# Optimization experiments

Measured on AMD Instinct MI355X. Metric: run time of the kernel, lower is better.

Reference implementation:

```python
import jax, jax.numpy as jnp
import numpy as np

SOFTCAP = 30.0

def setup_inputs() -> dict:
    key = jax.random.key(0)
    ks = jax.random.split(key, 5)
    T, D, F, E = 8192, 2048, 4096, 8
    s_in = 1.0 / np.sqrt(D)
    s_mid = 1.0 / np.sqrt(F)
    return {
        "hidden_states": jax.random.normal(ks[0], (T, D), jnp.float32),
        "gate_w": jax.random.normal(ks[1], (D, E), jnp.float32) * s_in,
        "w_gate": jax.random.normal(ks[2], (E, D, F), jnp.float32) * s_in,
        "w_up": jax.random.normal(ks[3], (E, D, F), jnp.float32) * s_in,
        "w_down": jax.random.normal(ks[4], (E, F, D), jnp.float32) * s_mid,
        "top_k": 2,
    }

def reference(hidden_states, gate_w, w_gate, w_up, w_down, top_k):
    x = hidden_states
    T = x.shape[0]
    # --- router: fp32 gate, tanh softcap, softmax ---
    logits = x.astype(jnp.float32) @ gate_w                      # [T, E]
    logits = jnp.tanh(logits / SOFTCAP) * SOFTCAP
    probs = jax.nn.softmax(logits, axis=-1)                      # [T, E]
    # --- top-k selection (weights are the softmax probs, no renorm) ---
    weights, idx = jax.lax.top_k(probs, top_k)                   # [T, k]
    combine = jnp.zeros_like(probs).at[jnp.arange(T)[:, None], idx].set(
        weights.astype(probs.dtype))                              # [T, E]
    combine = combine.astype(x.dtype)
    # --- expert MLPs: gelu(x@w_gate) * (x@w_up) @ w_down, scan over E ---
    def step(acc, ewts):
        wg, wu, wd, c = ewts                                     # [D,F],[D,F],[F,D],[T]
        h = jax.nn.gelu(x @ wg) * (x @ wu)                       # [T, F]
        return acc + c[:, None] * (h @ wd), None
    out, _ = jax.lax.scan(step, jnp.zeros_like(x),
                          (w_gate, w_up, w_down, combine.T))
    return out
```

## Files before the change

kernel.cpp:

```cpp
#include <hip/hip_runtime.h>
#include <hip/hip_bf16.h>
#include <cstdint>
#include <cstddef>

#define TNUM 8192
#define DDIM 2048
#define FDIM 4096
#define NEXP 8

typedef __attribute__((ext_vector_type(4))) float f32x4;
typedef __attribute__((ext_vector_type(4))) unsigned u32x4;
typedef __attribute__((ext_vector_type(8))) short s16x8;
typedef __attribute__((ext_vector_type(8))) __bf16 bf16x8v;

__device__ inline f32x4 mfma16(s16x8 a, s16x8 b, f32x4 c) {
  return __builtin_amdgcn_mfma_f32_16x16x32_bf16(
      __builtin_bit_cast(bf16x8v, a), __builtin_bit_cast(bf16x8v, b), c, 0, 0, 0);
}

__device__ inline unsigned short bf16r(float f) {
  union { float f; unsigned u; } x; x.f = f;
  unsigned r = x.u + 0x7fffu + ((x.u >> 16) & 1u);
  return (unsigned short)(r >> 16);
}

__device__ inline unsigned pk2(float a, float b) {
  __hip_bfloat162 h = __float22bfloat162_rn(make_float2(a, b));
  unsigned r;
  __builtin_memcpy(&r, &h, 4);
  return r;
}

typedef const __attribute__((address_space(1))) void* gp_t;
typedef __attribute__((address_space(3))) void* lp_t;
__device__ inline void gl16(const void* g, void* l) {
  __builtin_amdgcn_global_load_lds((gp_t)g, (lp_t)l, 16, 0, 0);
}

#define FENCE asm volatile("" ::: "memory")

__global__ __launch_bounds__(256) void k_router(
    const float* __restrict__ x, const float* __restrict__ gw,
    int* __restrict__ top_idx, float* __restrict__ top_w, int* __restrict__ counts) {
  __shared__ float gwT[NEXP][DDIM];
  const int tid = threadIdx.x;
  for (int i = tid; i < NEXP * DDIM; i += 256) {
    int d = i >> 3, e = i & 7;
    gwT[e][d] = gw[i];
  }
  __syncthreads();
  const int lane = tid & 63;
  const int t = blockIdx.x * 4 + (tid >> 6);
  const float4* xr = (const float4*)(x + (size_t)t * DDIM);
  double acc[NEXP];
#pragma unroll
  for (int e = 0; e < NEXP; e++) acc[e] = 0.0;
  for (int d4 = lane; d4 < DDIM / 4; d4 += 64) {
    float4 xv = xr[d4];
#pragma unroll
    for (int e = 0; e < NEXP; e++) {
      float4 gv = *(const float4*)&gwT[e][d4 * 4];
      acc[e] += (double)xv.x * gv.x + (double)xv.y * gv.y +
                (double)xv.z * gv.z + (double)xv.w * gv.w;
    }
  }
#pragma unroll
  for (int e = 0; e < NEXP; e++) {
    double v = acc[e];
#pragma unroll
    for (int s = 32; s > 0; s >>= 1) v += __shfl_xor(v, s);
    acc[e] = v;
  }
  if (lane == 0) {
    int i0 = 0; double b0 = acc[0];
#pragma unroll
    for (int e = 1; e < NEXP; e++) if (acc[e] > b0) { b0 = acc[e]; i0 = e; }
    int i1 = (i0 == 0) ? 1 : 0; double b1 = acc[i1];
#pragma unroll
    for (int e = 0; e < NEXP; e++) {
      if (e == i0 || e == i1) continue;
      if (acc[e] > b1) { b1 = acc[e]; i1 = e; }
    }
    float lc[NEXP]; float mx = -1e30f;
#pragma unroll
    for (int e = 0; e < NEXP; e++) {
      lc[e] = tanhf((float)(acc[e] * (1.0 / 30.0))) * 30.0f;
      mx = lc[e] > mx ? lc[e] : mx;
    }
    float s = 0.0f;
#pragma unroll
    for (int e = 0; e < NEXP; e++) { lc[e] = expf(lc[e] - mx); s += lc[e]; }
    float inv = 1.0f / s;
    top_idx[t * 2] = i0; top_idx[t * 2 + 1] = i1;
    top_w[t * 2] = lc[i0] * inv; top_w[t * 2 + 1] = lc[i1] * inv;
    atomicAdd(&counts[i0], 1);
    atomicAdd(&counts[i1], 1);
  }
}

__global__ void k_scan(const int* __restrict__ counts, int* __restrict__ offs,
                       int* __restrict__ cursor) {
  if (threadIdx.x == 0) {
    int s = 0;
    for (int e = 0; e < NEXP; e++) { offs[e] = s; cursor[e] = s; s += counts[e]; }
    offs[NEXP] = s;
  }
}

__global__ void k_scatter(const int* __restrict__ top_idx, const float* __restrict__ top_w,
                          int* __restrict__ cursor, int* __restrict__ perm_tok,
                          float* __restrict__ perm_w) {
  int t = blockIdx.x * 256 + threadIdx.x;
#pragma unroll
  for (int k = 0; k < 2; k++) {
    int e = top_idx[t * 2 + k];
    int pos = atomicAdd(&cursor[e], 1);
    perm_tok[pos] = t;
    perm_w[pos] = top_w[t * 2 + k];
  }
}

__global__ void k_cast(const float* __restrict__ x, unsigned short* __restrict__ xb) {
  size_t i = ((size_t)blockIdx.x * 256 + threadIdx.x) * 8;
  f32x4 a = *(const f32x4*)(x + i);
  f32x4 b = *(const f32x4*)(x + i + 4);
  u32x4 v;
  v[0] = pk2(a[0], a[1]); v[1] = pk2(a[2], a[3]);
  v[2] = pk2(b[0], b[1]); v[3] = pk2(b[2], b[3]);
  *(u32x4*)(xb + i) = v;
}

__global__ __launch_bounds__(256) void k_convT(
    const float* __restrict__ src, unsigned short* __restrict__ dst,
    int K, int N, int cmap) {
  __shared__ char ct[8192];
  const int e = blockIdx.z;
  const float* src_e = src + (size_t)e * K * N;
  const int nout = cmap ? 2 * N : N;
  unsigned short* dst_e = dst + (size_t)e * nout * K;
  const int k0 = blockIdx.y * 64, n0 = blockIdx.x * 64;
  const int tid = threadIdx.x;
#pragma unroll
  for (int i = 0; i < 4; i++) {
    int idx = tid + i * 256;
    int kr = idx >> 4, f4 = idx & 15;
    f32x4 v = *(const f32x4*)(src_e + (size_t)(k0 + kr) * N + n0 + f4 * 4);
#pragma unroll
    for (int j = 0; j < 4; j++) {
      int n = f4 * 4 + j;
      *(unsigned short*)(ct + n * 128 + ((kr * 2) ^ ((n & 7) << 4))) = bf16r(v[j]);
    }
  }
  __syncthreads();
#pragma unroll
  for (int i = 0; i < 2; i++) {
    int s = tid + i * 256;
    int n = s >> 3, ks = s & 7;
    int gn = n0 + n;
    int cd = cmap ? (((gn >> 4) << 5) + (gn & 15) + (cmap == 2 ? 16 : 0)) : gn;
    s16x8 val = *(const s16x8*)(ct + n * 128 + ((ks * 16) ^ ((n & 7) << 4)));
    *(s16x8*)(dst_e + (size_t)cd * K + k0 + ks * 8) = val;
  }
}

#define STG_A(KK, TN)                                                          \
  {                                                                            \
    char* d_ = lds + ((TN) & 1) * 65536 + (KK) * 16384 + wid * 2048;           \
    gl16(spA[0] + (size_t)(TN) * 128 + (KK) * 64, d_);                         \
    gl16(spA[1] + (size_t)(TN) * 128 + (KK) * 64, d_ + 1024);                  \
  }
#define STG_B(KK, TN)                                                          \
  {                                                                            \
    char* d_ = lds + ((TN) & 1) * 65536 + 32768 + (KK) * 16384 + wid * 2048;   \
    gl16(spB[0] + (size_t)(TN) * 128 + (KK) * 64, d_);                         \
    gl16(spB[1] + (size_t)(TN) * 128 + (KK) * 64, d_ + 1024);                  \
  }

#define VMC(N) asm volatile("s_waitcnt vmcnt(" #N ")" ::: "memory")

#define RGN(KK, TN, MORE)                                                      \
  {                                                                            \
    char* Aq_ = lds + ((TN) & 1) * 65536 + (KK) * 16384;                       \
    char* Bq_ = Aq_ + 32768;                                                   \
    s16x8 a_[8];                                                               \
    _Pragma("unroll") for (int mi = 0; mi < 8; mi++)                           \
      a_[mi] = *(const s16x8*)(Aq_ + (wr * 128 + mi * 16 + l15) * 64 + sl16);  \
    s16x8 b0_ = *(const s16x8*)(Bq_ + (wc * 64 + l15) * 64 + sl16);            \
    s16x8 b1_ = *(const s16x8*)(Bq_ + (wc * 64 + 16 + l15) * 64 + sl16);       \
    if (MORE) { STG_A(KK, (TN) + 1); }                                         \
    __builtin_amdgcn_s_setprio(1);                                             \
    _Pragma("unroll") for (int mi = 0; mi < 8; mi++) {                         \
      acc[mi][0] = mfma16(a_[mi], b0_, acc[mi][0]);                            \
      acc[mi][1] = mfma16(a_[mi], b1_, acc[mi][1]);                            \
    }                                                                          \
    __builtin_amdgcn_s_setprio(0);                                             \
    s16x8 b2_ = *(const s16x8*)(Bq_ + (wc * 64 + 32 + l15) * 64 + sl16);       \
    s16x8 b3_ = *(const s16x8*)(Bq_ + (wc * 64 + 48 + l15) * 64 + sl16);       \
    if (MORE) { STG_B(KK, (TN) + 1); }                                         \
    __builtin_amdgcn_s_setprio(1);                                             \
    _Pragma("unroll") for (int mi = 0; mi < 8; mi++) {                         \
      acc[mi][2] = mfma16(a_[mi], b2_, acc[mi][2]);                            \
      acc[mi][3] = mfma16(a_[mi], b3_, acc[mi][3]);                            \
    }                                                                          \
    __builtin_amdgcn_s_setprio(0);                                             \
  }

__global__ __launch_bounds__(512, 2) void k_mlp1(
    const unsigned short* __restrict__ xb, const unsigned short* __restrict__ wguT,
    const int* __restrict__ perm_tok, const int* __restrict__ offs,
    unsigned short* __restrict__ H) {
  extern __shared__ char lds[];
  const int e = blockIdx.z;
  const int off = offs[e], cnt = offs[e + 1] - off;
  const int nb = blockIdx.x * 256;
  const unsigned short* wgu_e = wguT + (size_t)e * 2 * DDIM * FDIM;
  const int tid = threadIdx.x;
  const int lane = tid & 63;
  const int wid = tid >> 6;
  const int wr = wid >> 2, wc = wid & 3;
  const int l15 = lane & 15, lk = lane >> 4;
  const int sl16 = (lk ^ ((l15 >> 1) & 3)) * 16;
  const int g16 = ((lane & 3) ^ ((lane >> 3) & 3)) * 16;
  const int NT = DDIM / 64;

#pragma unroll 1
  for (int mt = blockIdx.y; mt * 256 < cnt; mt += 8) {
    const char* spA[2];
    const char* spB[2];
#pragma unroll
    for (int c = 0; c < 2; c++) {
      int r = wid * 32 + c * 16 + (lane >> 2);
      int gm = mt * 256 + r;
      if (gm >= cnt) gm = cnt - 1;
      spA[c] = (const char*)(xb + (size_t)perm_tok[off + gm] * DDIM) + g16;
      spB[c] = (const char*)(wgu_e + (size_t)(nb + r) * DDIM) + g16;
    }
    f32x4 acc[8][4];
#pragma unroll
    for (int mi = 0; mi < 8; mi++)
#pragma unroll
      for (int ni = 0; ni < 4; ni++) acc[mi][ni] = f32x4{0.f, 0.f, 0.f, 0.f};

    STG_A(0, 0) STG_B(0, 0) STG_A(1, 0) STG_B(1, 0)
#pragma unroll 1
    for (int t = 0; t < NT; t++) {
      const bool more = (t + 1) < NT;
      VMC(4);
      FENCE;
      __builtin_amdgcn_s_barrier();
      FENCE;
      RGN(0, t, more)
      if (more) { VMC(4); } else { VMC(0); }
      FENCE;
      __builtin_amdgcn_s_barrier();
      FENCE;
      RGN(1, t, more)
    }

#pragma unroll
    for (int am = 0; am < 8; am++) {
      int rb = wr * 128 + am * 16 + lk * 4;
#pragma unroll
      for (int j = 0; j < 4; j++) {
        int gm = mt * 256 + rb + j;
        if (gm < cnt) {
          unsigned short* hrow = H + (size_t)(off + gm) * FDIM;
#pragma unroll
          for (int ni = 0; ni < 4; ni += 2) {
            int jj = (nb >> 4) + wc * 4 + ni;
            int hc = ((jj >> 1) << 4) + l15;
            float g = acc[am][ni][j];
            float u = acc[am][ni + 1][j];
            float x3 = g * g * g;
            float gl = 0.5f * g * (1.0f + tanhf(0.7978845608f * (g + 0.044715f * x3)));
            hrow[hc] = bf16r(gl * u);
          }
        }
      }
    }
  }
}

__global__ __launch_bounds__(512, 2) void k_mlp2(
    const unsigned short* __restrict__ H, const unsigned short* __restrict__ wdT,
    const int* __restrict__ perm_tok, const float* __restrict__ perm_w,
    const int* __restrict__ offs, float* __restrict__ out) {
  extern __shared__ char lds[];
  const int e = blockIdx.z;
  const int off = offs[e], cnt = offs[e + 1] - off;
  const int nb = blockIdx.x * 256;
  const unsigned short* wd_e = wdT + (size_t)e * FDIM * DDIM;
  const int tid = threadIdx.x;
  const int lane = tid & 63;
  const int wid = tid >> 6;
  const int wr = wid >> 2, wc = wid & 3;
  const int l15 = lane & 15, lk = lane >> 4;
  const int sl16 = (lk ^ ((l15 >> 1) & 3)) * 16;
  const int g16 = ((lane & 3) ^ ((lane >> 3) & 3)) * 16;
  const int NT = FDIM / 64;

#pragma unroll 1
  for (int mt = blockIdx.y; mt * 256 < cnt; mt += 8) {
    const char* spA[2];
    const char* spB[2];
#pragma unroll
    for (int c = 0; c < 2; c++) {
      int r = wid * 32 + c * 16 + (lane >> 2);
      int gm = mt * 256 + r;
      if (gm >= cnt) gm = cnt - 1;
      spA[c] = (const char*)(H + (size_t)(off + gm) * FDIM) + g16;
      spB[c] = (const char*)(wd_e + (size_t)(nb + r) * FDIM) + g16;
    }
    f32x4 acc[8][4];
#pragma unroll
    for (int mi = 0; mi < 8; mi++)
#pragma unroll
      for (int ni = 0; ni < 4; ni++) acc[mi][ni] = f32x4{0.f, 0.f, 0.f, 0.f};

    STG_A(0, 0) STG_B(0, 0) STG_A(1, 0) STG_B(1, 0)
#pragma unroll 1
    for (int t = 0; t < NT; t++) {
      const bool more = (t + 1) < NT;
      VMC(4);
      FENCE;
      __builtin_amdgcn_s_barrier();
      FENCE;
      RGN(0, t, more)
      if (more) { VMC(4); } else { VMC(0); }
      FENCE;
      __builtin_amdgcn_s_barrier();
      FENCE;
      RGN(1, t, more)
    }

#pragma unroll
    for (int am = 0; am < 8; am++) {
      int rb = wr * 128 + am * 16 + lk * 4;
#pragma unroll
      for (int j = 0; j < 4; j++) {
        int gm = mt * 256 + rb + j;
        if (gm < cnt) {
          int tok = perm_tok[off + gm];
          float w = perm_w[off + gm];
          float* orow = out + (size_t)tok * DDIM + nb + wc * 64 + l15;
#pragma unroll
          for (int ni = 0; ni < 4; ni++) atomicAdd(&orow[ni * 16], w * acc[am][ni][j]);
        }
      }
    }
  }
}

extern "C" void kernel_launch(void* const* d_in, const int* in_sizes, int n_in,
                              void* d_out, int out_size, void* d_ws, size_t ws_size,
                              hipStream_t stream) {
  const float* x = (const float*)d_in[0];
  const float* gw = (const float*)d_in[1];
  const float* wgate = (const float*)d_in[2];
  const float* wup = (const float*)d_in[3];
  const float* wdown = (const float*)d_in[4];
  float* out = (float*)d_out;

  const size_t XB_B = 33554432;
  const size_t H_B = 134217728;
  const size_t WGU_B = 268435456;
  const size_t WD_B = 134217728;

  char* ws = (char*)d_ws;
  unsigned short* xb = (unsigned short*)ws;
  unsigned short* H = (unsigned short*)(ws + XB_B);
  unsigned short* wguT = (unsigned short*)(ws + XB_B + H_B);
  unsigned short* wdT = (unsigned short*)(ws + XB_B + H_B + WGU_B);
  char* meta = ws + XB_B + H_B + WGU_B + WD_B;
  int* counts = (int*)(meta);
  int* offs = (int*)(meta + 64);
  int* cursor = (int*)(meta + 128);
  int* top_idx = (int*)(meta + 256);
  float* top_w = (float*)(meta + 256 + 65536);
  int* perm_tok = (int*)(meta + 256 + 131072);
  float* perm_w = (float*)(meta + 256 + 196608);

  (void)hipFuncSetAttribute((const void*)k_mlp1,
                            hipFuncAttributeMaxDynamicSharedMemorySize, 131072);
  (void)hipFuncSetAttribute((const void*)k_mlp2,
                            hipFuncAttributeMaxDynamicSharedMemorySize, 131072);

  (void)hipMemsetAsync(counts, 0, 64, stream);
  (void)hipMemsetAsync(d_out, 0, (size_t)TNUM * DDIM * 4, stream);
  k_router<<<TNUM / 4, 256, 0, stream>>>(x, gw, top_idx, top_w, counts);
  k_scan<<<1, 64, 0, stream>>>(counts, offs, cursor);
  k_scatter<<<TNUM / 256, 256, 0, stream>>>(top_idx, top_w, cursor, perm_tok, perm_w);
  k_cast<<<(TNUM * DDIM / 8) / 256, 256, 0, stream>>>(x, xb);
  k_convT<<<dim3(FDIM / 64, DDIM / 64, NEXP), 256, 0, stream>>>(wgate, wguT, DDIM, FDIM, 1);
  k_convT<<<dim3(FDIM / 64, DDIM / 64, NEXP), 256, 0, stream>>>(wup, wguT, DDIM, FDIM, 2);
  k_convT<<<dim3(DDIM / 64, FDIM / 64, NEXP), 256, 0, stream>>>(wdown, wdT, FDIM, DDIM, 0);
  k_mlp1<<<dim3(2 * FDIM / 256, 8, NEXP), 512, 131072, stream>>>(xb, wguT, perm_tok, offs, H);
  k_mlp2<<<dim3(DDIM / 256, 8, NEXP), 512, 131072, stream>>>(H, wdT, perm_tok, perm_w, offs, out);
}
```

Before: 1.468 ms.

## Restructure GEMM k-loop into ping-pong phases with half-tile A reads

Reworks the shared k-loop of both expert GEMM kernels into four phases per k-tile. Each phase reads half of the A fragments plus the B fragments, issues the next global-to-LDS stage, and runs a 4x4 MFMA block between barriers. The intent is a ping-pong schedule where the two waves per SIMD alternate memory and MFMA phases, while holding fewer A registers live. It adds many more barriers per iteration, which could stall if the waves do not interleave well. Correctness depends on the vmcnt waits still covering the staged buffers.

```diff
diff --git a/kernel.cpp b/kernel.cpp
--- a/kernel.cpp
+++ b/kernel.cpp
@@ -177,33 +177,48 @@
   }
 
 #define VMC(N) asm volatile("s_waitcnt vmcnt(" #N ")" ::: "memory")
-
-#define RGN(KK, TN, MORE)                                                      \
-  {                                                                            \
-    char* Aq_ = lds + ((TN) & 1) * 65536 + (KK) * 16384;                       \
-    char* Bq_ = Aq_ + 32768;                                                   \
-    s16x8 a_[8];                                                               \
-    _Pragma("unroll") for (int mi = 0; mi < 8; mi++)                           \
-      a_[mi] = *(const s16x8*)(Aq_ + (wr * 128 + mi * 16 + l15) * 64 + sl16);  \
-    s16x8 b0_ = *(const s16x8*)(Bq_ + (wc * 64 + l15) * 64 + sl16);            \
-    s16x8 b1_ = *(const s16x8*)(Bq_ + (wc * 64 + 16 + l15) * 64 + sl16);       \
-    if (MORE) { STG_A(KK, (TN) + 1); }                                         \
+#define BAR()  do { FENCE; __builtin_amdgcn_s_barrier(); FENCE; } while (0)
+
+#define RD_A(MIH, KK, TN)                                                      \
+    _Pragma("unroll") for (int mi = 0; mi < 4; mi++)                           \
+      a_[mi] = *(const s16x8*)(lds + ((TN) & 1) * 65536 + (KK) * 16384 +       \
+               (wr * 128 + (MIH) * 64 + mi * 16 + l15) * 64 + sl16);
+#define RD_B(KK, TN)                                                           \
+    _Pragma("unroll") for (int ni = 0; ni < 4; ni++)                           \
+      b_[ni] = *(const s16x8*)(lds + ((TN) & 1) * 65536 + 32768 +              \
+               (KK) * 16384 + (wc * 64 + ni * 16 + l15) * 64 + sl16);
+#define MM(MIH)                                                                \
     __builtin_amdgcn_s_setprio(1);                                             \
-    _Pragma("unroll") for (int mi = 0; mi < 8; mi++) {                         \
-      acc[mi][0] = mfma16(a_[mi], b0_, acc[mi][0]);                            \
-      acc[mi][1] = mfma16(a_[mi], b1_, acc[mi][1]);                            \
-    }                                                                          \
-    __builtin_amdgcn_s_setprio(0);                                             \
-    s16x8 b2_ = *(const s16x8*)(Bq_ + (wc * 64 + 32 + l15) * 64 + sl16);       \
-    s16x8 b3_ = *(const s16x8*)(Bq_ + (wc * 64 + 48 + l15) * 64 + sl16);       \
-    if (MORE) { STG_B(KK, (TN) + 1); }                                         \
-    __builtin_amdgcn_s_setprio(1);                                             \
-    _Pragma("unroll") for (int mi = 0; mi < 8; mi++) {                         \
-      acc[mi][2] = mfma16(a_[mi], b2_, acc[mi][2]);                            \
-      acc[mi][3] = mfma16(a_[mi], b3_, acc[mi][3]);                            \
-    }                                                                          \
-    __builtin_amdgcn_s_setprio(0);                                             \
-  }
+    _Pragma("unroll") for (int mi = 0; mi < 4; mi++)                           \
+      _Pragma("unroll") for (int ni = 0; ni < 4; ni++)                         \
+        acc[(MIH) * 4 + mi][ni] =                                              \
+            mfma16(a_[mi], b_[ni], acc[(MIH) * 4 + mi][ni]);                   \
+    __builtin_amdgcn_s_setprio(0);
+
+#define KLOOP(NT)                                                              \
+    STG_A(0, 0) STG_B(0, 0) STG_A(1, 0) STG_B(1, 0)                            \
+    VMC(4);                                                                    \
+    BAR();                                                                     \
+    _Pragma("unroll 1") for (int t = 0; t < (NT); t++) {                       \
+      const bool more = (t + 1) < (NT);                                        \
+      s16x8 a_[4], b_[4];                                                      \
+                                                         \
+      RD_A(0, 0, t) RD_B(0, t)                                                 \
+      if (more) { STG_A(0, t + 1); }                                           \
+      BAR(); MM(0) BAR();                                                      \
+                                                         \
+      RD_A(1, 0, t)                                                            \
+      if (more) { STG_B(0, t + 1); VMC(4); } else { VMC(0); }                  \
+      BAR(); MM(1) BAR();                                                      \
+                                                         \
+      RD_A(0, 1, t) RD_B(1, t)                                                 \
+      if (more) { STG_A(1, t + 1); }                                           \
+      BAR(); MM(0) BAR();                                                      \
+                                                         \
+      RD_A(1, 1, t)                                                            \
+      if (more) { STG_B(1, t + 1); VMC(4); } else { VMC(0); }                  \
+      BAR(); MM(1) BAR();                                                      \
+    }
 
 __global__ __launch_bounds__(512, 2) void k_mlp1(
     const unsigned short* __restrict__ xb, const unsigned short* __restrict__ wguT,
@@ -241,21 +256,7 @@
 #pragma unroll
       for (int ni = 0; ni < 4; ni++) acc[mi][ni] = f32x4{0.f, 0.f, 0.f, 0.f};
 
-    STG_A(0, 0) STG_B(0, 0) STG_A(1, 0) STG_B(1, 0)
-#pragma unroll 1
-    for (int t = 0; t < NT; t++) {
-      const bool more = (t + 1) < NT;
-      VMC(4);
-      FENCE;
-      __builtin_amdgcn_s_barrier();
-      FENCE;
-      RGN(0, t, more)
-      if (more) { VMC(4); } else { VMC(0); }
-      FENCE;
-      __builtin_amdgcn_s_barrier();
-      FENCE;
-      RGN(1, t, more)
-    }
+    KLOOP(NT)
 
 #pragma unroll
     for (int am = 0; am < 8; am++) {
@@ -317,21 +318,7 @@
 #pragma unroll
       for (int ni = 0; ni < 4; ni++) acc[mi][ni] = f32x4{0.f, 0.f, 0.f, 0.f};
 
-    STG_A(0, 0) STG_B(0, 0) STG_A(1, 0) STG_B(1, 0)
-#pragma unroll 1
-    for (int t = 0; t < NT; t++) {
-      const bool more = (t + 1) < NT;
-      VMC(4);
-      FENCE;
-      __builtin_amdgcn_s_barrier();
-      FENCE;
-      RGN(0, t, more)
-      if (more) { VMC(4); } else { VMC(0); }
-      FENCE;
-      __builtin_amdgcn_s_barrier();
-      FENCE;
-      RGN(1, t, more)
-    }
+    KLOOP(NT)
 
 #pragma unroll
     for (int am = 0; am < 8; am++) {
```

Result: slower. 1.538 ms (+4.7%).
